# Optimization experiments

Hardware: AMD Instinct MI355X
Metric: run time of the kernel (lower is better)

Reference implementation:

```python
import jax, jax.numpy as jnp
import numpy as np

EPS = 1e-5

def conv3x3(x, w, b):
    # x: [B,C,H,W], w: [O,I,3,3] -> SAME padding (pad=1)
    y = jax.lax.conv_general_dilated(x, w, (1, 1), 'SAME',
                                     dimension_numbers=('NCHW', 'OIHW', 'NCHW'))
    return y + b[None, :, None, None]

def batchnorm(x, g, b):
    # training-mode batch statistics over (B,H,W), biased variance (torch default)
    m = x.mean(axis=(0, 2, 3), keepdims=True)
    v = x.var(axis=(0, 2, 3), keepdims=True)
    return (x - m) / jnp.sqrt(v + EPS) * g[None, :, None, None] + b[None, :, None, None]

def setup_inputs() -> dict:
    key = jax.random.key(0)
    ks = jax.random.split(key, 24)
    B, Cin, Cout, T, H, W = 16, 256, 256, 256, 32, 32
    Cq = Cout // 8
    s = lambda fan: 1.0 / np.sqrt(fan)
    inp = {
        'x': jax.random.normal(ks[0], (B, Cin, H, W), jnp.float32),
        't': jax.random.normal(ks[1], (B, T), jnp.float32),
        # time_mlp: Linear(T,T) -> ReLU -> Linear(T,Cout)
        'w_t1': jax.random.normal(ks[2], (T, T), jnp.float32) * s(T),
        'b_t1': jax.random.normal(ks[3], (T,), jnp.float32) * s(T),
        'w_t2': jax.random.normal(ks[4], (Cout, T), jnp.float32) * s(T),
        'b_t2': jax.random.normal(ks[5], (Cout,), jnp.float32) * s(T),
        # convs (3x3, pad=1)
        'w_c1': jax.random.normal(ks[6], (Cout, Cin, 3, 3), jnp.float32) * s(Cin * 9),
        'b_c1': jax.random.normal(ks[7], (Cout,), jnp.float32) * s(Cin * 9),
        'w_c2': jax.random.normal(ks[8], (Cout, Cout, 3, 3), jnp.float32) * s(Cout * 9),
        'b_c2': jax.random.normal(ks[9], (Cout,), jnp.float32) * s(Cout * 9),
        'w_tr': jax.random.normal(ks[10], (Cout, Cout, 3, 3), jnp.float32) * s(Cout * 9),
        'b_tr': jax.random.normal(ks[11], (Cout,), jnp.float32) * s(Cout * 9),
        # batchnorm affine params
        'bn1_g': jnp.ones((Cout,), jnp.float32),
        'bn1_b': jnp.zeros((Cout,), jnp.float32),
        'bn2_g': jnp.ones((Cout,), jnp.float32),
        'bn2_b': jnp.zeros((Cout,), jnp.float32),
        # self-attention 1x1 convs (stored as [O,I])
        'wq': jax.random.normal(ks[12], (Cq, Cout), jnp.float32) * s(Cout),
        'bq': jax.random.normal(ks[13], (Cq,), jnp.float32) * s(Cout),
        'wk': jax.random.normal(ks[14], (Cq, Cout), jnp.float32) * s(Cout),
        'bk': jax.random.normal(ks[15], (Cq,), jnp.float32) * s(Cout),
        'wv': jax.random.normal(ks[16], (Cout, Cout), jnp.float32) * s(Cout),
        'bv': jax.random.normal(ks[17], (Cout,), jnp.float32) * s(Cout),
        # gamma is nn.Parameter(zeros(1)); use a random value so the residual branch is exercised
        'gamma': jax.random.normal(ks[18], (1,), jnp.float32),
    }
    return inp

def reference(x, t, w_t1, b_t1, w_t2, b_t2, w_c1, b_c1, w_c2, b_c2, w_tr, b_tr,
              bn1_g, bn1_b, bn2_g, bn2_b, wq, bq, wk, bk, wv, bv, gamma):
    # --- Block ---
    h = batchnorm(jax.nn.relu(conv3x3(x, w_c1, b_c1)), bn1_g, bn1_b)
    te = jax.nn.relu(t @ w_t1.T + b_t1)
    te = jax.nn.relu(te @ w_t2.T + b_t2)          # [B, Cout]
    h = h + te[:, :, None, None]
    h = batchnorm(jax.nn.relu(conv3x3(h, w_c2, b_c2)), bn2_g, bn2_b)
    y = conv3x3(h, w_tr, b_tr)                    # transform (up=False)
    # --- SelfAttention ---
    B, C, H, W = y.shape
    yf = y.reshape(B, C, H * W)                   # [B, C, N]
    Q = jnp.einsum('qc,bcn->bnq', wq, yf) + bq[None, None, :]   # [B, N, Cq]
    K = jnp.einsum('qc,bcn->bqn', wk, yf) + bk[None, :, None]   # [B, Cq, N]
    V = jnp.einsum('vc,bcn->bvn', wv, yf) + bv[None, :, None]   # [B, C, N]
    attn = jax.nn.softmax(jnp.einsum('bnq,bqm->bnm', Q, K), axis=-1)  # [B, N, N]
    out = jnp.einsum('bcm,bnm->bcn', V, attn).reshape(B, C, H, W)
    return gamma[0] * out + y
```

## Files before the change

### kernel.cpp

```cpp
#include <hip/hip_runtime.h>
#include <hip/hip_bf16.h>

using bf16 = __hip_bfloat16;

typedef __attribute__((ext_vector_type(8))) short bf16x8_t;
typedef __attribute__((ext_vector_type(4))) float f32x4_t;

__device__ __forceinline__ float b2f(bf16 x){ return __bfloat162float(x); }
__device__ __forceinline__ bf16  f2b(float x){ return __float2bfloat16(x); }
__device__ __forceinline__ unsigned short f2bu(float x){ bf16 h = __float2bfloat16(x); return *(unsigned short*)&h; }
__device__ __forceinline__ float bits2f(unsigned int lo16){ return __uint_as_float(lo16 << 16); }

__device__ __forceinline__ void gload16(const void* g, void* l) {
    __builtin_amdgcn_global_load_lds(
        (const __attribute__((address_space(1))) unsigned int*)g,
        (__attribute__((address_space(3))) unsigned int*)l, 16, 0, 0);
}


__global__ __launch_bounds__(256) void prep_all_k(
    const float* __restrict__ x, bf16* __restrict__ Xp0, bf16* __restrict__ Xp1,
    float* __restrict__ sums,
    const float* __restrict__ t, const float* __restrict__ w_t1, const float* __restrict__ b_t1,
    const float* __restrict__ w_t2, const float* __restrict__ b_t2, float* __restrict__ te,
    const float* __restrict__ w1, const float* __restrict__ w2, const float* __restrict__ w3,
    bf16* __restrict__ W1, bf16* __restrict__ W2, bf16* __restrict__ W3o,
    const float* __restrict__ wq, const float* __restrict__ wk, const float* __restrict__ wv,
    bf16* __restrict__ WQK, bf16* __restrict__ WVb)
{
    __shared__ char smem[64 * 65 * 4];
    const int blk = blockIdx.x;
    const int tid = threadIdx.x;

    if (blk < 1024) {
        float (*xs)[65] = (float(*)[65])smem;
        if (blk == 0) {
            sums[tid] = 0.f; sums[tid + 256] = 0.f; sums[tid + 512] = 0.f; sums[tid + 768] = 0.f;
        }
        const int b = blk >> 6, ct = (blk >> 4) & 3, nt = blk & 15;
        const int c0 = ct << 6, n0 = nt << 6;
        {
            const int cl = tid >> 2, nc = (tid & 3) << 4;
            const float* src = x + (size_t)((b << 8) + c0 + cl) * 1024 + n0 + nc;
            #pragma unroll
            for (int j = 0; j < 16; j += 4) {
                const float4 v = *(const float4*)(src + j);
                xs[cl][nc + j] = v.x; xs[cl][nc + j + 1] = v.y;
                xs[cl][nc + j + 2] = v.z; xs[cl][nc + j + 3] = v.w;
            }
        }
        __syncthreads();
        {
            const int nl = tid >> 2, cc = (tid & 3) << 4;
            const int n = n0 + nl;
            const int p = ((n >> 5) + 1) * 34 + (n & 31) + 1;
            unsigned int u[8];
            #pragma unroll
            for (int k = 0; k < 8; ++k)
                u[k] = (unsigned int)f2bu(xs[cc + 2 * k][nl]) | ((unsigned int)f2bu(xs[cc + 2 * k + 1][nl]) << 16);
            bf16* dst = Xp0 + (size_t)(b * 1156 + p) * 256 + c0 + cc;
            *(uint4*)dst = make_uint4(u[0], u[1], u[2], u[3]);
            *(uint4*)(dst + 8) = make_uint4(u[4], u[5], u[6], u[7]);
        }
    } else if (blk < 1792) {
        float* ls = (float*)smem;
        const int id = blk - 1024;
        const int co = id & 255;
        const int sel = id >> 8;
        const float* w = (sel == 0) ? w1 : (sel == 1) ? w2 : w3;
        bf16* dst = (sel == 0) ? W1 : (sel == 1) ? W2 : W3o;
        const float* src = w + (size_t)co * 2304;
        #pragma unroll
        for (int i = 0; i < 9; ++i) ls[tid + (i << 8)] = src[tid + (i << 8)];
        __syncthreads();
        #pragma unroll
        for (int off = 0; off < 9; ++off)
            dst[(size_t)(co * 9 + off) * 256 + tid] = f2b(ls[tid * 9 + off]);
    } else if (blk < 2112) {
        const int r = blk - 1792;
        if (r < 32)       WQK[r * 256 + tid] = f2b(wq[r * 256 + tid]);
        else if (r < 64)  WQK[r * 256 + tid] = f2b(wk[(r - 32) * 256 + tid]);
        else              WVb[(r - 64) * 256 + tid] = f2b(wv[(r - 64) * 256 + tid]);
    } else if (blk < 2128) {
        float* tr = (float*)smem;
        float* hid = tr + 256;
        const int b = blk - 2112, j = tid;
        tr[j] = t[(b << 8) + j];
        __syncthreads();
        float s = b_t1[j];
        const float* wp = w_t1 + j * 256;
        for (int k = 0; k < 256; ++k) s += tr[k] * wp[k];
        hid[j] = fmaxf(s, 0.f);
        __syncthreads();
        float s2 = b_t2[j];
        const float* wp2 = w_t2 + j * 256;
        for (int k = 0; k < 256; ++k) s2 += hid[k] * wp2[k];
        te[(b << 8) + j] = fmaxf(s2, 0.f);
    } else {
        const int idx = (blk - 2128) * 256 + tid;
        const int v = idx >> 6;
        const int o = (idx & 63) << 1;
        if (v < 4224) {
            const int buf = v / 2112;
            const int rem = v - buf * 2112;
            const int b = rem / 132;
            const int h = rem - b * 132;
            int p;
            if (h < 34)        p = h;
            else if (h < 68)   p = 1122 + (h - 34);
            else if (h < 100)  p = (h - 68 + 1) * 34;
            else               p = (h - 100 + 1) * 34 + 33;
            unsigned int* dst = (unsigned int*)((buf ? Xp1 : Xp0) + (size_t)(b * 1156 + p) * 256);
            dst[o] = 0u; dst[o + 1] = 0u;
        }
    }
}

template<bool RELU, bool STATS>
__global__ __launch_bounds__(512, 1) void conv_mfma_k(
    const bf16* __restrict__ Xp, const bf16* __restrict__ W3,
    const float* __restrict__ bias, bf16* __restrict__ outp, float* __restrict__ sums)
{
    __shared__ bf16 Als[3][128 * 64];
    __shared__ bf16 Bls[3][128 * 64];
    __shared__ float sstat[256];
    const int tid = threadIdx.x;
    const int wid = tid >> 6, lane = tid & 63;
    const int wm = wid >> 2, wn = wid & 3;
    const int blk = blockIdx.x;
    const int xc = blk & 7, tt = blk >> 3;
    const int b = xc + ((tt >> 4) << 3);
    const int tile = tt & 15, mt = tile >> 1, nt = tile & 1;
    const int m0 = mt << 7, co0 = nt << 7;

    if (STATS && tid < 256) sstat[tid] = 0.f;

    const int lrow = tid >> 3;
    const int sL8 = (((tid & 7) ^ (lrow & 7)) << 3);

    const bf16* agp[2]; const bf16* bgp[2];
    #pragma unroll
    for (int i = 0; i < 2; ++i) {
        const int r = (i << 6) + lrow;
        const int n = m0 + r;
        const int pb = (n >> 5) * 34 + (n & 31);
        agp[i] = Xp + (size_t)(b * 1156 + pb) * 256 + sL8;
        bgp[i] = W3 + (size_t)(co0 + r) * 2304 + sL8;
    }

    const int rsel = lane & 15;
    const int s0 = (((lane >> 4) ^ (lane & 7)) << 3);
    const int s1 = ((((lane >> 4) + 4) ^ (lane & 7)) << 3);
    const int abase = ((wm << 6) + rsel) << 6;
    const int bbase = ((wn << 5) + rsel) << 6;

    f32x4_t acc[4][2];
    #pragma unroll
    for (int mi = 0; mi < 4; ++mi)
        #pragma unroll
        for (int ni = 0; ni < 2; ++ni)
            acc[mi][ni] = (f32x4_t){0.f, 0.f, 0.f, 0.f};

    auto STAGE = [&](int kt2, int buf) {
        const int off_ = kt2 >> 2, cic_ = kt2 & 3;
        const int kh_ = (off_ * 11) >> 5;
        const int doff_ = ((off_ + 31 * kh_) << 8) + (cic_ << 6);
        const int koff_ = (off_ << 8) + (cic_ << 6);
        #pragma unroll
        for (int i = 0; i < 2; ++i) {
            gload16(agp[i] + doff_, &Als[buf][((i << 6) + (wid << 3)) << 6]);
            gload16(bgp[i] + koff_, &Bls[buf][((i << 6) + (wid << 3)) << 6]);
        }
    };

    STAGE(0, 0); STAGE(1, 1);
    for (int kt = 0; kt < 36; ++kt) {
        if (kt < 35) asm volatile("s_waitcnt vmcnt(4)" ::: "memory");
        else         asm volatile("s_waitcnt vmcnt(0)" ::: "memory");
        __builtin_amdgcn_s_barrier();
        asm volatile("" ::: "memory");
        const int cur = kt % 3;
        #pragma unroll
        for (int kh = 0; kh < 2; ++kh) {
            const int sk = kh ? s1 : s0;
            bf16x8_t av[4], bv[2];
            #pragma unroll
            for (int mi = 0; mi < 4; ++mi)
                av[mi] = *(const bf16x8_t*)(&Als[cur][abase + (mi << 10) + sk]);
            #pragma unroll
            for (int ni = 0; ni < 2; ++ni)
                bv[ni] = *(const bf16x8_t*)(&Bls[cur][bbase + (ni << 10) + sk]);
            #pragma unroll
            for (int mi = 0; mi < 4; ++mi)
                #pragma unroll
                for (int ni = 0; ni < 2; ++ni)
                    acc[mi][ni] = __builtin_amdgcn_mfma_f32_16x16x32_bf16(
                        av[mi], bv[ni], acc[mi][ni], 0, 0, 0);
        }
        if (kt + 2 < 36) STAGE(kt + 2, (kt + 2) % 3);
    }

    const int cr = (lane >> 4) << 2;
    const int cc = lane & 15;
    #pragma unroll
    for (int ni = 0; ni < 2; ++ni) {
        const int co = co0 + (wn << 5) + (ni << 4) + cc;
        const float bb = bias[co];
        float ssum = 0.f, ssq = 0.f;
        #pragma unroll
        for (int mi = 0; mi < 4; ++mi) {
            const int n = m0 + (wm << 6) + (mi << 4) + cr;
            #pragma unroll
            for (int j = 0; j < 4; ++j) {
                float v = acc[mi][ni][j] + bb;
                if (RELU) v = fmaxf(v, 0.f);
                outp[(size_t)((b << 10) + n + j) * 256 + co] = f2b(v);
                if (STATS) { ssum += v; ssq += v * v; }
            }
        }
        if (STATS) {
            ssum += __shfl_xor(ssum, 16); ssum += __shfl_xor(ssum, 32);
            ssq  += __shfl_xor(ssq, 16);  ssq  += __shfl_xor(ssq, 32);
            if (lane < 16) {
                const int ch = (wn << 5) + (ni << 4) + cc;
                atomicAdd(&sstat[ch * 2], ssum);
                atomicAdd(&sstat[ch * 2 + 1], ssq);
            }
        }
    }
    if (STATS) {
        __syncthreads();
        if (tid < 128) {
            atomicAdd(&sums[co0 + tid], sstat[tid * 2]);
            atomicAdd(&sums[256 + co0 + tid], sstat[tid * 2 + 1]);
        }
    }
}

template<bool TE>
__global__ __launch_bounds__(256) void bn_apply_T_k(
    const bf16* __restrict__ a, const float* __restrict__ sums,
    const float* __restrict__ g, const float* __restrict__ bb,
    const float* __restrict__ te, bf16* __restrict__ Xp)
{
    const int t = threadIdx.x;
    const int row = blockIdx.x * 8 + (t >> 5);
    const int c0 = (t & 31) << 3;
    const int b = row >> 10, n = row & 1023;
    const uint4 u = *(const uint4*)(a + (size_t)row * 256 + c0);
    const unsigned int w[4] = {u.x, u.y, u.z, u.w};
    float scv[8], shv[8];
    #pragma unroll
    for (int k = 0; k < 8; ++k) {
        const int c = c0 + k;
        const float m = sums[c] * (1.f / 16384.f);
        const float var = sums[256 + c] * (1.f / 16384.f) - m * m;
        const float sc = g[c] * rsqrtf(var + 1e-5f);
        scv[k] = sc;
        shv[k] = bb[c] - m * sc + (TE ? te[(b << 8) + c] : 0.f);
    }
    unsigned int o[4];
    #pragma unroll
    for (int k = 0; k < 4; ++k) {
        const float v0 = bits2f(w[k] & 0xffffu) * scv[2*k] + shv[2*k];
        const float v1 = __uint_as_float(w[k] & 0xffff0000u) * scv[2*k+1] + shv[2*k+1];
        o[k] = (unsigned int)f2bu(v0) | ((unsigned int)f2bu(v1) << 16);
    }
    const int p = ((n >> 5) + 1) * 34 + (n & 31) + 1;
    *(uint4*)(Xp + (size_t)(b * 1156 + p) * 256 + c0) = make_uint4(o[0], o[1], o[2], o[3]);
}

__global__ __launch_bounds__(512, 1) void qkv_mfma_k(
    const bf16* __restrict__ WVb, const bf16* __restrict__ Yt,
    const float* __restrict__ bvp, bf16* __restrict__ Vb,
    const bf16* __restrict__ WQK, const float* __restrict__ bq,
    const float* __restrict__ bk, bf16* __restrict__ QKb)
{
    __shared__ bf16 Als[3][128 * 64];
    __shared__ bf16 Bls[3][128 * 64];
    const int tid = threadIdx.x;
    const int wid = tid >> 6, lane = tid & 63;

    if (blockIdx.x >= 256) {
        const int blk2 = blockIdx.x - 256;
        const int b = blk2 >> 3, m0 = (blk2 & 7) << 7;
        const int n0w = m0 + (wid << 4);
        const bf16* arow = Yt + (size_t)((b << 10) + n0w + (lane & 15)) * 256 + ((lane >> 4) << 3);
        const int boff = ((lane >> 4) << 3);
        f32x4_t acc[4];
        #pragma unroll
        for (int ni = 0; ni < 4; ++ni) acc[ni] = (f32x4_t){0.f,0.f,0.f,0.f};
        for (int k0 = 0; k0 < 256; k0 += 32) {
            const bf16x8_t av = *(const bf16x8_t*)(arow + k0);
            #pragma unroll
            for (int ni = 0; ni < 4; ++ni) {
                const bf16x8_t bv = *(const bf16x8_t*)(WQK + (ni * 16 + (lane & 15)) * 256 + k0 + boff);
                acc[ni] = __builtin_amdgcn_mfma_f32_16x16x32_bf16(av, bv, acc[ni], 0, 0, 0);
            }
        }
        const int cr = (lane >> 4) << 2, cc = lane & 15;
        #pragma unroll
        for (int ni = 0; ni < 4; ++ni) {
            const int q = ni * 16 + cc;
            const float bias = (q < 32) ? bq[q] : bk[q - 32];
            #pragma unroll
            for (int j = 0; j < 4; ++j) {
                const int n = n0w + cr + j;
                QKb[(size_t)((b << 10) + n) * 64 + q] = f2b(acc[ni][j] + bias);
            }
        }
        return;
    }

    const int wm = wid >> 2, wn = wid & 3;
    const int blk = blockIdx.x;
    const int xc = blk & 7, tt = blk >> 3;
    const int b = xc + ((tt >> 4) << 3);
    const int tile = tt & 15, vt = tile >> 3, nt = tile & 7;
    const int v0 = vt << 7, n0 = nt << 7;

    const int lrow = tid >> 3;
    const int sL8 = (((tid & 7) ^ (lrow & 7)) << 3);
    const bf16* agp[2]; const bf16* bgp[2];
    #pragma unroll
    for (int i = 0; i < 2; ++i) {
        const int r = (i << 6) + lrow;
        agp[i] = WVb + (size_t)(v0 + r) * 256 + sL8;
        bgp[i] = Yt + (size_t)((b << 10) + n0 + r) * 256 + sL8;
    }
    const int rsel = lane & 15;
    const int s0 = (((lane >> 4) ^ (lane & 7)) << 3);
    const int s1 = ((((lane >> 4) + 4) ^ (lane & 7)) << 3);
    const int abase = ((wm << 6) + rsel) << 6;
    const int bbase = ((wn << 5) + rsel) << 6;

    f32x4_t acc[4][2];
    #pragma unroll
    for (int mi = 0; mi < 4; ++mi)
        #pragma unroll
        for (int ni = 0; ni < 2; ++ni)
            acc[mi][ni] = (f32x4_t){0.f,0.f,0.f,0.f};

    auto STAGE = [&](int kt2, int buf) {
        const int koff = kt2 << 6;
        #pragma unroll
        for (int i = 0; i < 2; ++i) {
            gload16(agp[i] + koff, &Als[buf][((i << 6) + (wid << 3)) << 6]);
            gload16(bgp[i] + koff, &Bls[buf][((i << 6) + (wid << 3)) << 6]);
        }
    };

    STAGE(0, 0); STAGE(1, 1);
    for (int kt = 0; kt < 4; ++kt) {
        if (kt < 3) asm volatile("s_waitcnt vmcnt(4)" ::: "memory");
        else        asm volatile("s_waitcnt vmcnt(0)" ::: "memory");
        __builtin_amdgcn_s_barrier();
        asm volatile("" ::: "memory");
        const int cur = kt % 3;
        #pragma unroll
        for (int kh = 0; kh < 2; ++kh) {
            const int sk = kh ? s1 : s0;
            bf16x8_t av[4], bv[2];
            #pragma unroll
            for (int mi = 0; mi < 4; ++mi)
                av[mi] = *(const bf16x8_t*)(&Als[cur][abase + (mi << 10) + sk]);
            #pragma unroll
            for (int ni = 0; ni < 2; ++ni)
                bv[ni] = *(const bf16x8_t*)(&Bls[cur][bbase + (ni << 10) + sk]);
            #pragma unroll
            for (int mi = 0; mi < 4; ++mi)
                #pragma unroll
                for (int ni = 0; ni < 2; ++ni)
                    acc[mi][ni] = __builtin_amdgcn_mfma_f32_16x16x32_bf16(
                        av[mi], bv[ni], acc[mi][ni], 0, 0, 0);
        }
        if (kt + 2 < 4) STAGE(kt + 2, (kt + 2) % 3);
    }

    const int cr = (lane >> 4) << 2, cc = lane & 15;
    #pragma unroll
    for (int mi = 0; mi < 4; ++mi) {
        #pragma unroll
        for (int j = 0; j < 4; ++j) {
            const int v = v0 + (wm << 6) + (mi << 4) + cr + j;
            const float bb = bvp[v];
            #pragma unroll
            for (int ni = 0; ni < 2; ++ni) {
                const int n = n0 + (wn << 5) + (ni << 4) + cc;
                Vb[(size_t)((b << 8) + v) * 1024 + n] = f2b(acc[mi][ni][j] + bb);
            }
        }
    }
}

__global__ __launch_bounds__(256) void softmax_k(
    const bf16* __restrict__ QKb, bf16* __restrict__ P, float* __restrict__ invs)
{
    const int b = blockIdx.x >> 5, n0 = (blockIdx.x & 31) << 5;
    const int tid = threadIdx.x, wid = tid >> 6, lane = tid & 63;
    const int m0w = wid << 8;
    __shared__ float wred[4][32];

    const bf16* qbase = QKb + (size_t)((b << 10) + n0) * 64;
    const int koff = (lane >> 4) << 3;
    bf16x8_t qf[2];
    #pragma unroll
    for (int nt = 0; nt < 2; ++nt)
        qf[nt] = *(const bf16x8_t*)(qbase + (nt * 16 + (lane & 15)) * 64 + koff);
    const bf16* kbase = QKb + (size_t)(b << 10) * 64 + 32;

    float mx[2] = {-3.0e38f, -3.0e38f};
    for (int mi = 0; mi < 16; ++mi) {
        const bf16x8_t kf = *(const bf16x8_t*)(kbase + (m0w + mi * 16 + (lane & 15)) * 64 + koff);
        #pragma unroll
        for (int nt = 0; nt < 2; ++nt) {
            f32x4_t s = (f32x4_t){0.f,0.f,0.f,0.f};
            s = __builtin_amdgcn_mfma_f32_16x16x32_bf16(kf, qf[nt], s, 0, 0, 0);
            mx[nt] = fmaxf(mx[nt], fmaxf(fmaxf(s[0], s[1]), fmaxf(s[2], s[3])));
        }
    }
    #pragma unroll
    for (int nt = 0; nt < 2; ++nt) {
        mx[nt] = fmaxf(mx[nt], __shfl_xor(mx[nt], 16));
        mx[nt] = fmaxf(mx[nt], __shfl_xor(mx[nt], 32));
        if (lane < 16) wred[wid][nt * 16 + lane] = mx[nt];
    }
    __syncthreads();
    float rm[2];
    #pragma unroll
    for (int nt = 0; nt < 2; ++nt) {
        const int c = nt * 16 + (lane & 15);
        rm[nt] = fmaxf(fmaxf(wred[0][c], wred[1][c]), fmaxf(wred[2][c], wred[3][c]));
    }
    __syncthreads();

    float sm[2] = {0.f, 0.f};
    for (int mi = 0; mi < 16; ++mi) {
        const bf16x8_t kf = *(const bf16x8_t*)(kbase + (m0w + mi * 16 + (lane & 15)) * 64 + koff);
        #pragma unroll
        for (int nt = 0; nt < 2; ++nt) {
            f32x4_t s = (f32x4_t){0.f,0.f,0.f,0.f};
            s = __builtin_amdgcn_mfma_f32_16x16x32_bf16(kf, qf[nt], s, 0, 0, 0);
            const float p0 = __expf(s[0] - rm[nt]);
            const float p1 = __expf(s[1] - rm[nt]);
            const float p2 = __expf(s[2] - rm[nt]);
            const float p3 = __expf(s[3] - rm[nt]);
            sm[nt] += (p0 + p1) + (p2 + p3);
            uint2 u;
            u.x = (unsigned int)f2bu(p0) | ((unsigned int)f2bu(p1) << 16);
            u.y = (unsigned int)f2bu(p2) | ((unsigned int)f2bu(p3) << 16);
            const int n = n0 + nt * 16 + (lane & 15);
            const int m = m0w + mi * 16 + ((lane >> 4) << 2);
            *(uint2*)(P + (size_t)((b << 10) + n) * 1024 + m) = u;
        }
    }
    #pragma unroll
    for (int nt = 0; nt < 2; ++nt) {
        sm[nt] += __shfl_xor(sm[nt], 16);
        sm[nt] += __shfl_xor(sm[nt], 32);
        if (lane < 16) wred[wid][nt * 16 + lane] = sm[nt];
    }
    __syncthreads();
    if (tid < 32) {
        const float total = wred[0][tid] + wred[1][tid] + wred[2][tid] + wred[3][tid];
        invs[(b << 10) + n0 + tid] = 1.f / total;
    }
}

__global__ __launch_bounds__(512, 1) void pv_mfma_k(
    const bf16* __restrict__ Vb, const bf16* __restrict__ P,
    const float* __restrict__ invs, const bf16* __restrict__ Yt,
    const float* __restrict__ gamma, float* __restrict__ out)
{
    __shared__ bf16 Als[3][128 * 64];
    __shared__ bf16 Bls[3][128 * 64];
    const int tid = threadIdx.x;
    const int wid = tid >> 6, lane = tid & 63;
    const int wm = wid >> 2, wn = wid & 3;
    const int blk = blockIdx.x;
    const int xc = blk & 7, tt = blk >> 3;
    const int b = xc + ((tt >> 4) << 3);
    const int tile = tt & 15, ct = tile >> 3, nt = tile & 7;
    const int c0 = ct << 7, n0 = nt << 7;

    const int lrow = tid >> 3;
    const int sL8 = (((tid & 7) ^ (lrow & 7)) << 3);
    const bf16* agp[2]; const bf16* bgp[2];
    #pragma unroll
    for (int i = 0; i < 2; ++i) {
        const int r = (i << 6) + lrow;
        agp[i] = Vb + (size_t)((b << 8) + c0 + r) * 1024 + sL8;
        bgp[i] = P + (size_t)((b << 10) + n0 + r) * 1024 + sL8;
    }
    const int rsel = lane & 15;
    const int s0 = (((lane >> 4) ^ (lane & 7)) << 3);
    const int s1 = ((((lane >> 4) + 4) ^ (lane & 7)) << 3);
    const int abase = ((wm << 6) + rsel) << 6;
    const int bbase = ((wn << 5) + rsel) << 6;

    f32x4_t acc[4][2];
    #pragma unroll
    for (int mi = 0; mi < 4; ++mi)
        #pragma unroll
        for (int ni = 0; ni < 2; ++ni)
            acc[mi][ni] = (f32x4_t){0.f,0.f,0.f,0.f};

    auto STAGE = [&](int kt2, int buf) {
        const int koff = kt2 << 6;
        #pragma unroll
        for (int i = 0; i < 2; ++i) {
            gload16(agp[i] + koff, &Als[buf][((i << 6) + (wid << 3)) << 6]);
            gload16(bgp[i] + koff, &Bls[buf][((i << 6) + (wid << 3)) << 6]);
        }
    };

    STAGE(0, 0); STAGE(1, 1);
    for (int kt = 0; kt < 16; ++kt) {
        if (kt < 15) asm volatile("s_waitcnt vmcnt(4)" ::: "memory");
        else         asm volatile("s_waitcnt vmcnt(0)" ::: "memory");
        __builtin_amdgcn_s_barrier();
        asm volatile("" ::: "memory");
        const int cur = kt % 3;
        #pragma unroll
        for (int kh = 0; kh < 2; ++kh) {
            const int sk = kh ? s1 : s0;
            bf16x8_t av[4], bv[2];
            #pragma unroll
            for (int mi = 0; mi < 4; ++mi)
                av[mi] = *(const bf16x8_t*)(&Als[cur][abase + (mi << 10) + sk]);
            #pragma unroll
            for (int ni = 0; ni < 2; ++ni)
                bv[ni] = *(const bf16x8_t*)(&Bls[cur][bbase + (ni << 10) + sk]);
            #pragma unroll
            for (int mi = 0; mi < 4; ++mi)
                #pragma unroll
                for (int ni = 0; ni < 2; ++ni)
                    acc[mi][ni] = __builtin_amdgcn_mfma_f32_16x16x32_bf16(
                        av[mi], bv[ni], acc[mi][ni], 0, 0, 0);
        }
        if (kt + 2 < 16) STAGE(kt + 2, (kt + 2) % 3);
    }

    const float g = gamma[0];
    const int cr = (lane >> 4) << 2, cc = lane & 15;
    #pragma unroll
    for (int ni = 0; ni < 2; ++ni) {
        const int n = n0 + (wn << 5) + (ni << 4) + cc;
        const float gi = g * invs[(b << 10) + n];
        #pragma unroll
        for (int mi = 0; mi < 4; ++mi) {
            const int c = c0 + (wm << 6) + (mi << 4) + cr;
            const bf16* yp = Yt + (size_t)((b << 10) + n) * 256 + c;
            #pragma unroll
            for (int j = 0; j < 4; ++j)
                out[(size_t)((b << 8) + c + j) * 1024 + n] = gi * acc[mi][ni][j] + b2f(yp[j]);
        }
    }
}

extern "C" void kernel_launch(void* const* d_in, const int* in_sizes, int n_in,
                              void* d_out, int out_size, void* d_ws, size_t ws_size,
                              hipStream_t stream)
{
    const float* x     = (const float*)d_in[0];
    const float* t     = (const float*)d_in[1];
    const float* w_t1  = (const float*)d_in[2];
    const float* b_t1  = (const float*)d_in[3];
    const float* w_t2  = (const float*)d_in[4];
    const float* b_t2  = (const float*)d_in[5];
    const float* w_c1  = (const float*)d_in[6];
    const float* b_c1  = (const float*)d_in[7];
    const float* w_c2  = (const float*)d_in[8];
    const float* b_c2  = (const float*)d_in[9];
    const float* w_tr  = (const float*)d_in[10];
    const float* b_tr  = (const float*)d_in[11];
    const float* bn1g  = (const float*)d_in[12];
    const float* bn1b  = (const float*)d_in[13];
    const float* bn2g  = (const float*)d_in[14];
    const float* bn2b  = (const float*)d_in[15];
    const float* wq    = (const float*)d_in[16];
    const float* bq    = (const float*)d_in[17];
    const float* wk    = (const float*)d_in[18];
    const float* bk    = (const float*)d_in[19];
    const float* wv    = (const float*)d_in[20];
    const float* bv    = (const float*)d_in[21];
    const float* gamma = (const float*)d_in[22];
    float* out = (float*)d_out;

    char* ws = (char*)d_ws;
    float* te    = (float*)(ws + 0);
    float* sums1 = (float*)(ws + 16384);
    float* sums2 = (float*)(ws + 18432);
    char* base = ws + 32768;
    bf16* W3_1 = (bf16*)(base);
    bf16* W3_2 = (bf16*)(base + 1179648);
    bf16* W3_3 = (bf16*)(base + 2359296);
    bf16* Xp0  = (bf16*)(base + 3538944);
    bf16* Xp1  = (bf16*)(base + 13008896);
    bf16* Craw = (bf16*)(base + 22478848);
    bf16* P    = (bf16*)(base);
    bf16* Yt   = (bf16*)(base + 33554432);
    bf16* QKb  = (bf16*)(base + 41943040);
    bf16* Vb   = (bf16*)(base + 44040192);
    float* invs= (float*)(base + 52428800);
    bf16* WQK  = (bf16*)(base + 52494336);
    bf16* WVb  = (bf16*)(base + 52527104);

    prep_all_k<<<3184, 256, 0, stream>>>(
        x, Xp0, Xp1, sums1,
        t, w_t1, b_t1, w_t2, b_t2, te,
        w_c1, w_c2, w_tr, W3_1, W3_2, W3_3,
        wq, wk, wv, WQK, WVb);

    conv_mfma_k<true, true><<<256, 512, 0, stream>>>(Xp0, W3_1, b_c1, Craw, sums1);
    bn_apply_T_k<true><<<2048, 256, 0, stream>>>(Craw, sums1, bn1g, bn1b, te, Xp1);

    conv_mfma_k<true, true><<<256, 512, 0, stream>>>(Xp1, W3_2, b_c2, Craw, sums2);
    bn_apply_T_k<false><<<2048, 256, 0, stream>>>(Craw, sums2, bn2g, bn2b, nullptr, Xp0);

    conv_mfma_k<false, false><<<256, 512, 0, stream>>>(Xp0, W3_3, b_tr, Yt, nullptr);

    qkv_mfma_k<<<384, 512, 0, stream>>>(WVb, Yt, bv, Vb, WQK, bq, bk, QKb);
    softmax_k<<<512, 256, 0, stream>>>(QKb, P, invs);
    pv_mfma_k<<<256, 512, 0, stream>>>(Vb, P, invs, Yt, gamma, out);
}
```

Baseline: 158.4 us.

## Stage a halo input slab per channel chunk and reuse it across all 3x3 taps

The 3x3 implicit-GEMM conv loop is reordered so the outer loop runs over 64-channel chunks and the inner loop over the 9 kernel taps. For each chunk, one padded 4x34-pixel halo slab of the input is loaded into LDS (double-buffered), and A fragments for every tap are read from that slab at shifted offsets, using an XOR swizzle to avoid bank conflicts. This replaces the earlier scheme that reloaded a 128-pixel A tile from global memory for every tap, cutting input traffic. Weight tiles stay triple-buffered, the 36-step loop is fully unrolled, and LDS use grows. The vmcnt(2) wait at the step before a new slab is needed also forces that slab's load to finish early, which may add a stall.

```diff
diff --git a/kernel.cpp b/kernel.cpp
--- a/kernel.cpp
+++ b/kernel.cpp
@@ -121,8 +121,8 @@
     const bf16* __restrict__ Xp, const bf16* __restrict__ W3,
     const float* __restrict__ bias, bf16* __restrict__ outp, float* __restrict__ sums)
 {
-    __shared__ bf16 Als[3][128 * 64];
-    __shared__ bf16 Bls[3][128 * 64];
+    __shared__ bf16 Als[2][16384];
+    __shared__ bf16 Bls[3][8192];
     __shared__ float sstat[256];
     const int tid = threadIdx.x;
     const int wid = tid >> 6, lane = tid & 63;
@@ -135,24 +135,26 @@
 
     if (STATS && tid < 256) sstat[tid] = 0.f;
 
+    const bf16* xsl = Xp + (size_t)(b * 1156 + mt * 136) * 256;
+
     const int lrow = tid >> 3;
     const int sL8 = (((tid & 7) ^ (lrow & 7)) << 3);
-
-    const bf16* agp[2]; const bf16* bgp[2];
-    #pragma unroll
-    for (int i = 0; i < 2; ++i) {
-        const int r = (i << 6) + lrow;
-        const int n = m0 + r;
-        const int pb = (n >> 5) * 34 + (n & 31);
-        agp[i] = Xp + (size_t)(b * 1156 + pb) * 256 + sL8;
-        bgp[i] = W3 + (size_t)(co0 + r) * 2304 + sL8;
-    }
-
-    const int rsel = lane & 15;
-    const int s0 = (((lane >> 4) ^ (lane & 7)) << 3);
-    const int s1 = ((((lane >> 4) + 4) ^ (lane & 7)) << 3);
-    const int abase = ((wm << 6) + rsel) << 6;
+    const bf16* bgp[2];
+    #pragma unroll
+    for (int i = 0; i < 2; ++i)
+        bgp[i] = W3 + (size_t)(co0 + (i << 6) + lrow) * 2304 + sL8;
+
+    const int apix = (wid << 3) + (lane >> 3);
+    const int aj0 = lane & 7;
+
+    const int rsel = lane & 15, lg = lane >> 4;
+    const int s0 = ((lg ^ (lane & 7)) << 3);
+    const int s1 = (((lg + 4) ^ (lane & 7)) << 3);
     const int bbase = ((wn << 5) + rsel) << 6;
+    int dbase[4];
+    #pragma unroll
+    for (int mi = 0; mi < 4; ++mi)
+        dbase[mi] = ((wm << 1) + (mi >> 1)) * 34 + ((mi & 1) << 4) + rsel;
 
     f32x4_t acc[4][2];
     #pragma unroll
@@ -161,35 +163,49 @@
         for (int ni = 0; ni < 2; ++ni)
             acc[mi][ni] = (f32x4_t){0.f, 0.f, 0.f, 0.f};
 
-    auto STAGE = [&](int kt2, int buf) {
-        const int off_ = kt2 >> 2, cic_ = kt2 & 3;
-        const int kh_ = (off_ * 11) >> 5;
-        const int doff_ = ((off_ + 31 * kh_) << 8) + (cic_ << 6);
-        const int koff_ = (off_ << 8) + (cic_ << 6);
-        #pragma unroll
-        for (int i = 0; i < 2; ++i) {
-            gload16(agp[i] + doff_, &Als[buf][((i << 6) + (wid << 3)) << 6]);
-            gload16(bgp[i] + koff_, &Bls[buf][((i << 6) + (wid << 3)) << 6]);
+    auto STAGE_A = [&](int cic, int buf) {
+        #pragma unroll
+        for (int i = 0; i < 4; ++i) {
+            const int pix = (i << 6) + apix;
+            const int j = aj0 ^ (pix & 7);
+            gload16(xsl + (size_t)pix * 256 + (cic << 6) + (j << 3),
+                    &Als[buf][((i << 9) + (wid << 6)) << 3]);
         }
     };
-
-    STAGE(0, 0); STAGE(1, 1);
-    for (int kt = 0; kt < 36; ++kt) {
-        if (kt < 35) asm volatile("s_waitcnt vmcnt(4)" ::: "memory");
+    auto STAGE_B = [&](int st, int buf) {
+        const int koff = ((st % 9) << 8) + ((st / 9) << 6);
+        #pragma unroll
+        for (int i = 0; i < 2; ++i)
+            gload16(bgp[i] + koff, &Bls[buf][((i << 6) + (wid << 3)) << 6]);
+    };
+
+    STAGE_A(0, 0);
+    STAGE_B(0, 0);
+    STAGE_B(1, 1);
+
+    #pragma unroll
+    for (int st = 0; st < 36; ++st) {
+        if (st < 35) asm volatile("s_waitcnt vmcnt(2)" ::: "memory");
         else         asm volatile("s_waitcnt vmcnt(0)" ::: "memory");
         __builtin_amdgcn_s_barrier();
         asm volatile("" ::: "memory");
-        const int cur = kt % 3;
+        const int cic = st / 9, off = st % 9;
+        const int doff = (off / 3) * 34 + (off % 3);
+        const bf16* abuf = Als[cic & 1];
+        const bf16* bbuf = Bls[st % 3];
         #pragma unroll
         for (int kh = 0; kh < 2; ++kh) {
             const int sk = kh ? s1 : s0;
             bf16x8_t av[4], bv[2];
             #pragma unroll
-            for (int mi = 0; mi < 4; ++mi)
-                av[mi] = *(const bf16x8_t*)(&Als[cur][abase + (mi << 10) + sk]);
+            for (int mi = 0; mi < 4; ++mi) {
+                const int sp = dbase[mi] + doff;
+                av[mi] = *(const bf16x8_t*)((const char*)abuf +
+                            (sp << 7) + ((((kh << 2) + lg) ^ (sp & 7)) << 4));
+            }
             #pragma unroll
             for (int ni = 0; ni < 2; ++ni)
-                bv[ni] = *(const bf16x8_t*)(&Bls[cur][bbase + (ni << 10) + sk]);
+                bv[ni] = *(const bf16x8_t*)(bbuf + bbase + (ni << 10) + sk);
             #pragma unroll
             for (int mi = 0; mi < 4; ++mi)
                 #pragma unroll
@@ -197,11 +213,12 @@
                     acc[mi][ni] = __builtin_amdgcn_mfma_f32_16x16x32_bf16(
                         av[mi], bv[ni], acc[mi][ni], 0, 0, 0);
         }
-        if (kt + 2 < 36) STAGE(kt + 2, (kt + 2) % 3);
-    }
-
-    const int cr = (lane >> 4) << 2;
-    const int cc = lane & 15;
+        if (st + 2 < 36) STAGE_B(st + 2, (st + 2) % 3);
+        if (off == 7 && st < 27) STAGE_A(cic + 1, (cic + 1) & 1);
+    }
+
+    const int cr = lg << 2;
+    const int cc = rsel;
     #pragma unroll
     for (int ni = 0; ni < 2; ++ni) {
         const int co = co0 + (wn << 5) + (ni << 4) + cc;
```

Measured after the change: 150.7 us. 4.9% less time.
